# Kernel optimization log

Hardware: AMD Instinct MI355X
Metric: run time of the kernel (lower is better)

Reference implementation:

```python
import jax, jax.numpy as jnp
import numpy as np

K = 16          # NUM_PARTS (foreground parts); K+1 prototypes incl. background
D = 768         # EMBED_DIM
C = 200         # NUM_CLASSES
LN_EPS = 1e-6


def setup_inputs() -> dict:
    key = jax.random.key(0)
    k1, k2, k3, k4 = jax.random.split(key, 4)
    B, H, W = 32, 24, 24
    patch_features = jax.random.normal(k1, (B, H, W, D), dtype=jnp.float32)
    prototypes = 0.02 * jax.random.normal(k2, (K + 1, D), dtype=jnp.float32)
    ln_gamma = jnp.ones((D,), dtype=jnp.float32)
    ln_beta = jnp.zeros((D,), dtype=jnp.float32)
    # keras Dense default: glorot_uniform kernel, zero bias
    lim = np.sqrt(6.0 / (D + C)).astype(np.float32)
    w_cls = jax.random.uniform(k3, (D, C), dtype=jnp.float32, minval=-lim, maxval=lim)
    b_cls = jnp.zeros((C,), dtype=jnp.float32)
    return {
        "patch_features": patch_features,
        "prototypes": prototypes,
        "ln_gamma": ln_gamma,
        "ln_beta": ln_beta,
        "w_cls": w_cls,
        "b_cls": b_cls,
    }


def reference(patch_features, prototypes, ln_gamma, ln_beta, w_cls, b_cls):
    B, H, W, Dm = patch_features.shape
    P = H * W
    x = patch_features.reshape(B, P, Dm)                      # (B,P,D)

    # squared euclidean distance to K+1 prototypes, expressed as a GEMM:
    # ||z - p||^2 = ||z||^2 - 2 z.p + ||p||^2   -> (B,P,K+1)
    x_sq = jnp.sum(x * x, axis=-1, keepdims=True)             # (B,P,1)
    p_sq = jnp.sum(prototypes * prototypes, axis=-1)          # (K+1,)
    xp = jnp.einsum("bpd,kd->bpk", x, prototypes)             # (B,P,K+1)
    dists = x_sq - 2.0 * xp + p_sq                            # (B,P,K+1)

    # eval path: plain softmax over -distances
    a = jax.nn.softmax(-dists, axis=-1)                       # (B,P,K+1)

    # attention maps (B, K+1, H, W)
    A = jnp.transpose(a, (0, 2, 1)).reshape(B, K + 1, H, W)

    # weighted aggregation of patch features per part, normalized by P
    v_all = jnp.einsum("bpk,bpd->bkd", a, x) / jnp.float32(P) # (B,K+1,D)
    v_fg = v_all[:, :K, :]                                    # (B,K,D)

    # layernorm over last axis (eps=1e-6, learnable gamma/beta)
    mu = jnp.mean(v_fg, axis=-1, keepdims=True)
    var = jnp.mean(jnp.square(v_fg - mu), axis=-1, keepdims=True)
    v_norm = (v_fg - mu) * jax.lax.rsqrt(var + LN_EPS) * ln_gamma + ln_beta

    # shared per-part classifier + mean aggregation over parts
    logits_parts = jnp.einsum("bkd,dc->bkc", v_norm, w_cls) + b_cls  # (B,K,C)
    logits_agg = jnp.mean(logits_parts, axis=1)                      # (B,C)

    return (A, v_norm, logits_parts, logits_agg)
```

## Files before the change

### kernel.cpp

```cpp
#include <hip/hip_runtime.h>
#include <hip/hip_bf16.h>

#define B    32
#define P    576
#define D    768
#define K1   17
#define KFG  16
#define C    200
#define LN_EPS 1e-6f

typedef __attribute__((ext_vector_type(8))) short short8;
typedef __attribute__((ext_vector_type(4))) float f32x4;

__device__ inline unsigned short f2b(float f) {
    union { float f; unsigned u; } x; x.f = f;
    unsigned r = x.u + 0x7FFF + ((x.u >> 16) & 1);
    return (unsigned short)(r >> 16);
}

__device__ inline short8 cvt8(float4 a, float4 b) {
    union { unsigned u[4]; short8 s; } r;
    union { __hip_bfloat162 h; unsigned u; } c;
    c.h = __float22bfloat162_rn(make_float2(a.x, a.y)); r.u[0] = c.u;
    c.h = __float22bfloat162_rn(make_float2(a.z, a.w)); r.u[1] = c.u;
    c.h = __float22bfloat162_rn(make_float2(b.x, b.y)); r.u[2] = c.u;
    c.h = __float22bfloat162_rn(make_float2(b.z, b.w)); r.u[3] = c.u;
    return r.s;
}

__global__ __launch_bounds__(256) void k_pre(const float* __restrict__ proto,
                                             float* __restrict__ psq,
                                             unsigned short* __restrict__ pbf) {
    const int k = blockIdx.x, t = threadIdx.x;
    float a0 = proto[k * D + t], a1 = proto[k * D + t + 256], a2 = proto[k * D + t + 512];
    pbf[k * D + t]       = f2b(a0);
    pbf[k * D + t + 256] = f2b(a1);
    pbf[k * D + t + 512] = f2b(a2);
    float s = a0 * a0 + a1 * a1 + a2 * a2;
    #pragma unroll
    for (int o = 1; o < 64; o <<= 1) s += __shfl_xor(s, o, 64);
    __shared__ float r[4];
    if ((t & 63) == 0) r[t >> 6] = s;
    __syncthreads();
    if (t == 0) psq[k] = r[0] + r[1] + r[2] + r[3];
}

__global__ __launch_bounds__(64, 2) void k_dots(const float* __restrict__ x,
                                                const unsigned short* __restrict__ pbf,
                                                const float* __restrict__ psq,
                                                float* __restrict__ A_out,
                                                float* __restrict__ apool) {
    const int tile = blockIdx.x, b = blockIdx.y;
    const int lane = threadIdx.x;
    const int n = lane & 15, kq = lane >> 4;
    const int p0 = tile * 16;

    const float*          arow = x   + ((size_t)(b * P + p0 + n)) * D + kq * 8;
    const unsigned short* brow = pbf + (size_t)n  * D + kq * 8;
    const unsigned short* brw6 = pbf + (size_t)16 * D + kq * 8;

    f32x4 acc0 = {0.f, 0.f, 0.f, 0.f};
    f32x4 acc1 = {0.f, 0.f, 0.f, 0.f};

    #pragma unroll 8
    for (int s = 0; s < 24; ++s) {
        const float* ap = arow + s * 32;
        float4 v0 = *(const float4*)(ap);
        float4 v1 = *(const float4*)(ap + 4);
        short8 A  = cvt8(v0, v1);
        short8 Bv = *(const short8*)(brow + s * 32);
        short8 B6 = *(const short8*)(brw6 + s * 32);
        acc0 = __builtin_amdgcn_mfma_f32_16x16x32_bf16(A, Bv, acc0, 0, 0, 0);
        acc1 = __builtin_amdgcn_mfma_f32_16x16x32_bf16(A, B6, acc1, 0, 0, 0);
    }

    const float pq = psq[n], pq16 = psq[16];
    float a_[4], a16[4];
    #pragma unroll
    for (int r = 0; r < 4; ++r) {
        float l0  = 2.f * acc0[r] - pq;
        float l16 = 2.f * acc1[r] - pq16;
        float mx = l0;
        #pragma unroll
        for (int o = 1; o < 16; o <<= 1) mx = fmaxf(mx, __shfl_xor(mx, o, 64));
        mx = fmaxf(mx, l16);
        float e0  = __expf(l0 - mx);
        float e16 = __expf(l16 - mx);
        float sum = e0;
        #pragma unroll
        for (int o = 1; o < 16; o <<= 1) sum += __shfl_xor(sum, o, 64);
        sum += e16;
        const float inv = 1.f / sum;
        a_[r]  = e0 * inv;
        a16[r] = e16 * inv;
    }

    *(float4*)(A_out + ((size_t)b * K1 + n) * P + p0 + kq * 4) =
        make_float4(a_[0], a_[1], a_[2], a_[3]);
    if (n == 0)
        *(float4*)(A_out + ((size_t)b * K1 + 16) * P + p0 + kq * 4) =
            make_float4(a16[0], a16[1], a16[2], a16[3]);

    const float invP = 1.f / (float)P;
    #pragma unroll
    for (int r = 0; r < 4; ++r)
        apool[((size_t)b * P + p0 + kq * 4 + r) * KFG + n] = a_[r] * invP;
}

__global__ __launch_bounds__(256, 4) void k_pool(const float* __restrict__ x,
                                                 const float* __restrict__ apool,
                                                 float* __restrict__ vpart) {
    const int dc = blockIdx.x, psl = blockIdx.y, b = blockIdx.z;
    const int t = threadIdx.x;
    const int d = dc * 256 + t;

    const float* aw = apool + ((size_t)b * P + psl * 96) * KFG;
    const float* xp = x + ((size_t)b * P + psl * 96) * D + d;

    float acc[KFG];
    #pragma unroll
    for (int k = 0; k < KFG; ++k) acc[k] = 0.f;

    #pragma unroll 4
    for (int p = 0; p < 96; ++p) {
        float xv = xp[(size_t)p * D];
        f32x4 A0 = *(const f32x4*)(aw + p * 16);
        f32x4 A1 = *(const f32x4*)(aw + p * 16 + 4);
        f32x4 A2 = *(const f32x4*)(aw + p * 16 + 8);
        f32x4 A3 = *(const f32x4*)(aw + p * 16 + 12);
        acc[0]  += A0[0] * xv; acc[1]  += A0[1] * xv; acc[2]  += A0[2] * xv; acc[3]  += A0[3] * xv;
        acc[4]  += A1[0] * xv; acc[5]  += A1[1] * xv; acc[6]  += A1[2] * xv; acc[7]  += A1[3] * xv;
        acc[8]  += A2[0] * xv; acc[9]  += A2[1] * xv; acc[10] += A2[2] * xv; acc[11] += A2[3] * xv;
        acc[12] += A3[0] * xv; acc[13] += A3[1] * xv; acc[14] += A3[2] * xv; acc[15] += A3[3] * xv;
    }
    float* o = vpart + ((size_t)(psl * B + b) * KFG) * D + d;
    #pragma unroll
    for (int k = 0; k < KFG; ++k) o[(size_t)k * D] = acc[k];
}

__global__ __launch_bounds__(256) void k_ln(const float* __restrict__ vpart,
                                            const float* __restrict__ gamma,
                                            const float* __restrict__ beta,
                                            float* __restrict__ vnorm_out,
                                            float* __restrict__ vT) {
    const int k = blockIdx.x, b = blockIdx.y, t = threadIdx.x;
    const int lane = t & 63, wv = t >> 6;

    float v[3]; float s1 = 0.f, s2 = 0.f;
    #pragma unroll
    for (int j = 0; j < 3; ++j) {
        const int d = t + j * 256;
        float s = 0.f;
        #pragma unroll
        for (int psl = 0; psl < 6; ++psl)
            s += vpart[((size_t)(psl * B + b) * KFG + k) * D + d];
        v[j] = s; s1 += s; s2 += s * s;
    }
    #pragma unroll
    for (int o = 1; o < 64; o <<= 1) {
        s1 += __shfl_xor(s1, o, 64);
        s2 += __shfl_xor(s2, o, 64);
    }
    __shared__ float r1[4], r2[4];
    if (lane == 0) { r1[wv] = s1; r2[wv] = s2; }
    __syncthreads();
    s1 = r1[0] + r1[1] + r1[2] + r1[3];
    s2 = r2[0] + r2[1] + r2[2] + r2[3];

    const float mean = s1 * (1.f / (float)D);
    const float var  = s2 * (1.f / (float)D) - mean * mean;
    const float rs   = rsqrtf(var + LN_EPS);

    #pragma unroll
    for (int j = 0; j < 3; ++j) {
        const int d = t + j * 256;
        float vn = (v[j] - mean) * rs * gamma[d] + beta[d];
        vnorm_out[((size_t)b * KFG + k) * D + d] = vn;
        vT[((size_t)b * D + d) * KFG + k] = vn;
    }
}

__global__ __launch_bounds__(256) void k_cls(const float* __restrict__ vT,
                                             const float* __restrict__ W,
                                             float* __restrict__ lpart) {
    const int dq = blockIdx.x, b = blockIdx.y;
    const int c = threadIdx.x;
    const int cc = c < C ? c : (C - 1);

    const float* vt = vT + ((size_t)b * D + dq * 96) * KFG;
    const float* Wp = W + (size_t)dq * 96 * C + cc;

    float acc[KFG];
    #pragma unroll
    for (int k = 0; k < KFG; ++k) acc[k] = 0.f;

    #pragma unroll 4
    for (int i = 0; i < 96; ++i) {
        float wl = Wp[(size_t)i * C];
        f32x4 V0 = *(const f32x4*)(vt + i * 16);
        f32x4 V1 = *(const f32x4*)(vt + i * 16 + 4);
        f32x4 V2 = *(const f32x4*)(vt + i * 16 + 8);
        f32x4 V3 = *(const f32x4*)(vt + i * 16 + 12);
        acc[0]  += V0[0] * wl; acc[1]  += V0[1] * wl; acc[2]  += V0[2] * wl; acc[3]  += V0[3] * wl;
        acc[4]  += V1[0] * wl; acc[5]  += V1[1] * wl; acc[6]  += V1[2] * wl; acc[7]  += V1[3] * wl;
        acc[8]  += V2[0] * wl; acc[9]  += V2[1] * wl; acc[10] += V2[2] * wl; acc[11] += V2[3] * wl;
        acc[12] += V3[0] * wl; acc[13] += V3[1] * wl; acc[14] += V3[2] * wl; acc[15] += V3[3] * wl;
    }
    if (c < C) {
        float* o = lpart + ((size_t)(dq * B + b) * KFG) * C + c;
        #pragma unroll
        for (int k = 0; k < KFG; ++k) o[(size_t)k * C] = acc[k];
    }
}

__global__ __launch_bounds__(256) void k_comb(const float* __restrict__ lpart,
                                              const float* __restrict__ bcls,
                                              float* __restrict__ parts,
                                              float* __restrict__ agg) {
    const int b = blockIdx.x, c = threadIdx.x;
    if (c >= C) return;
    const float bc = bcls[c];
    float s_agg = 0.f;
    #pragma unroll
    for (int k = 0; k < KFG; ++k) {
        float s = bc;
        #pragma unroll
        for (int dq = 0; dq < 8; ++dq)
            s += lpart[((size_t)(dq * B + b) * KFG + k) * C + c];
        parts[((size_t)b * KFG + k) * C + c] = s;
        s_agg += s;
    }
    agg[(size_t)b * C + c] = s_agg * (1.f / (float)KFG);
}

extern "C" void kernel_launch(void* const* d_in, const int* in_sizes, int n_in,
                              void* d_out, int out_size, void* d_ws, size_t ws_size,
                              hipStream_t stream) {
    const float* x     = (const float*)d_in[0];
    const float* proto = (const float*)d_in[1];
    const float* gamma = (const float*)d_in[2];
    const float* beta  = (const float*)d_in[3];
    const float* W     = (const float*)d_in[4];
    const float* bcls  = (const float*)d_in[5];

    float* out = (float*)d_out;
    float* A_out     = out;
    float* vnorm_out = out + 313344;
    float* parts_out = out + 706560;
    float* agg_out   = out + 808960;

    float* ws = (float*)d_ws;
    float* psq  = ws;
    unsigned short* pbf = (unsigned short*)(ws + 32);
    float* apool = ws + 32 + 6528;
    float* vpart = apool + 294912;
    float* vT    = vpart + 2359296;
    float* lpart = vT + 393216;

    hipLaunchKernelGGL(k_pre,  dim3(K1),        dim3(256), 0, stream, proto, psq, pbf);
    hipLaunchKernelGGL(k_dots, dim3(36, B),     dim3(64),  0, stream, x, pbf, psq, A_out, apool);
    hipLaunchKernelGGL(k_pool, dim3(3, 6, B),   dim3(256), 0, stream, x, apool, vpart);
    hipLaunchKernelGGL(k_ln,   dim3(KFG, B),    dim3(256), 0, stream, vpart, gamma, beta, vnorm_out, vT);
    hipLaunchKernelGGL(k_cls,  dim3(8, B),      dim3(256), 0, stream, vT, W, lpart);
    hipLaunchKernelGGL(k_comb, dim3(B),         dim3(256), 0, stream, lpart, bcls, parts_out, agg_out);
}
```

Baseline: 147.8 us.

## Fuse all stages into one cooperative persistent kernel with grid syncs

Replaces the six separate kernel launches with a single cooperative kernel of 256 blocks that runs each stage in turn, separated by grid-wide barriers. The pooling stage now splits P into 8 slices instead of 6, and the workspace layout grows to match. The aim is to remove the per-launch gaps and tail effects between small stages. In exchange, the grid holds only 256 blocks of 256 threads, one block per CU, so the dots and pooling phases run at much lower occupancy than the original launches, and every grid barrier adds its own cost.

```diff
diff --git a/kernel.cpp b/kernel.cpp
--- a/kernel.cpp
+++ b/kernel.cpp
@@ -1,5 +1,8 @@
 #include <hip/hip_runtime.h>
 #include <hip/hip_bf16.h>
+#include <hip/hip_cooperative_groups.h>
+
+namespace cg = cooperative_groups;
 
 #define B    32
 #define P    576
@@ -28,209 +31,227 @@
     return r.s;
 }
 
-__global__ __launch_bounds__(256) void k_pre(const float* __restrict__ proto,
-                                             float* __restrict__ psq,
-                                             unsigned short* __restrict__ pbf) {
-    const int k = blockIdx.x, t = threadIdx.x;
-    float a0 = proto[k * D + t], a1 = proto[k * D + t + 256], a2 = proto[k * D + t + 512];
-    pbf[k * D + t]       = f2b(a0);
-    pbf[k * D + t + 256] = f2b(a1);
-    pbf[k * D + t + 512] = f2b(a2);
-    float s = a0 * a0 + a1 * a1 + a2 * a2;
-    #pragma unroll
-    for (int o = 1; o < 64; o <<= 1) s += __shfl_xor(s, o, 64);
-    __shared__ float r[4];
-    if ((t & 63) == 0) r[t >> 6] = s;
-    __syncthreads();
-    if (t == 0) psq[k] = r[0] + r[1] + r[2] + r[3];
-}
-
-__global__ __launch_bounds__(64, 2) void k_dots(const float* __restrict__ x,
-                                                const unsigned short* __restrict__ pbf,
-                                                const float* __restrict__ psq,
-                                                float* __restrict__ A_out,
-                                                float* __restrict__ apool) {
-    const int tile = blockIdx.x, b = blockIdx.y;
-    const int lane = threadIdx.x;
-    const int n = lane & 15, kq = lane >> 4;
-    const int p0 = tile * 16;
-
-    const float*          arow = x   + ((size_t)(b * P + p0 + n)) * D + kq * 8;
-    const unsigned short* brow = pbf + (size_t)n  * D + kq * 8;
-    const unsigned short* brw6 = pbf + (size_t)16 * D + kq * 8;
-
-    f32x4 acc0 = {0.f, 0.f, 0.f, 0.f};
-    f32x4 acc1 = {0.f, 0.f, 0.f, 0.f};
-
-    #pragma unroll 8
-    for (int s = 0; s < 24; ++s) {
-        const float* ap = arow + s * 32;
-        float4 v0 = *(const float4*)(ap);
-        float4 v1 = *(const float4*)(ap + 4);
-        short8 A  = cvt8(v0, v1);
-        short8 Bv = *(const short8*)(brow + s * 32);
-        short8 B6 = *(const short8*)(brw6 + s * 32);
-        acc0 = __builtin_amdgcn_mfma_f32_16x16x32_bf16(A, Bv, acc0, 0, 0, 0);
-        acc1 = __builtin_amdgcn_mfma_f32_16x16x32_bf16(A, B6, acc1, 0, 0, 0);
-    }
-
-    const float pq = psq[n], pq16 = psq[16];
-    float a_[4], a16[4];
-    #pragma unroll
-    for (int r = 0; r < 4; ++r) {
-        float l0  = 2.f * acc0[r] - pq;
-        float l16 = 2.f * acc1[r] - pq16;
-        float mx = l0;
+__global__ __launch_bounds__(256, 1) void k_all(
+        const float* __restrict__ x, const float* __restrict__ proto,
+        const float* __restrict__ gamma, const float* __restrict__ beta,
+        const float* __restrict__ W, const float* __restrict__ bcls,
+        float* __restrict__ A_out, float* __restrict__ vnorm_out,
+        float* __restrict__ parts_out, float* __restrict__ agg_out,
+        float* __restrict__ psq, unsigned short* __restrict__ pbf,
+        float* __restrict__ apool, float* __restrict__ vpart,
+        float* __restrict__ vT, float* __restrict__ lpart) {
+    cg::grid_group grid = cg::this_grid();
+    __shared__ float sred[8];
+
+    const int gid = blockIdx.x, t = threadIdx.x;
+    const int wv = t >> 6, lane = t & 63;
+
+    if (gid < K1) {
+        const int k = gid;
+        float a0 = proto[k * D + t], a1 = proto[k * D + t + 256], a2 = proto[k * D + t + 512];
+        pbf[k * D + t]       = f2b(a0);
+        pbf[k * D + t + 256] = f2b(a1);
+        pbf[k * D + t + 512] = f2b(a2);
+        float s = a0 * a0 + a1 * a1 + a2 * a2;
         #pragma unroll
-        for (int o = 1; o < 16; o <<= 1) mx = fmaxf(mx, __shfl_xor(mx, o, 64));
-        mx = fmaxf(mx, l16);
-        float e0  = __expf(l0 - mx);
-        float e16 = __expf(l16 - mx);
-        float sum = e0;
+        for (int o = 1; o < 64; o <<= 1) s += __shfl_xor(s, o, 64);
+        if (lane == 0) sred[wv] = s;
+        __syncthreads();
+        if (t == 0) psq[k] = sred[0] + sred[1] + sred[2] + sred[3];
+    }
+    __threadfence();
+    grid.sync();
+
+    {
+        const int n = lane & 15, kq = lane >> 4;
+        for (int u = gid * 4 + wv; u < 1152; u += 1024) {
+            const int tile = u % 36, b = u / 36;
+            const int p0 = tile * 16;
+
+            const float*          arow = x   + ((size_t)(b * P + p0 + n)) * D + kq * 8;
+            const unsigned short* brow = pbf + (size_t)n  * D + kq * 8;
+            const unsigned short* brw6 = pbf + (size_t)16 * D + kq * 8;
+
+            f32x4 acc0 = {0.f, 0.f, 0.f, 0.f};
+            f32x4 acc1 = {0.f, 0.f, 0.f, 0.f};
+
+            #pragma unroll 8
+            for (int s = 0; s < 24; ++s) {
+                const float* ap = arow + s * 32;
+                float4 v0 = *(const float4*)(ap);
+                float4 v1 = *(const float4*)(ap + 4);
+                short8 A  = cvt8(v0, v1);
+                short8 Bv = *(const short8*)(brow + s * 32);
+                short8 B6 = *(const short8*)(brw6 + s * 32);
+                acc0 = __builtin_amdgcn_mfma_f32_16x16x32_bf16(A, Bv, acc0, 0, 0, 0);
+                acc1 = __builtin_amdgcn_mfma_f32_16x16x32_bf16(A, B6, acc1, 0, 0, 0);
+            }
+
+            const float pq = psq[n], pq16 = psq[16];
+            float a_[4], a16[4];
+            #pragma unroll
+            for (int r = 0; r < 4; ++r) {
+                float l0  = 2.f * acc0[r] - pq;
+                float l16 = 2.f * acc1[r] - pq16;
+                float mx = l0;
+                #pragma unroll
+                for (int o = 1; o < 16; o <<= 1) mx = fmaxf(mx, __shfl_xor(mx, o, 64));
+                mx = fmaxf(mx, l16);
+                float e0  = __expf(l0 - mx);
+                float e16 = __expf(l16 - mx);
+                float sum = e0;
+                #pragma unroll
+                for (int o = 1; o < 16; o <<= 1) sum += __shfl_xor(sum, o, 64);
+                sum += e16;
+                const float inv = 1.f / sum;
+                a_[r]  = e0 * inv;
+                a16[r] = e16 * inv;
+            }
+
+            *(float4*)(A_out + ((size_t)b * K1 + n) * P + p0 + kq * 4) =
+                make_float4(a_[0], a_[1], a_[2], a_[3]);
+            if (n == 0)
+                *(float4*)(A_out + ((size_t)b * K1 + 16) * P + p0 + kq * 4) =
+                    make_float4(a16[0], a16[1], a16[2], a16[3]);
+
+            const float invP = 1.f / (float)P;
+            #pragma unroll
+            for (int r = 0; r < 4; ++r)
+                apool[((size_t)b * P + p0 + kq * 4 + r) * KFG + n] = a_[r] * invP;
+        }
+    }
+    __threadfence();
+    grid.sync();
+    __threadfence();
+
+    {
+        for (int u = gid; u < 768; u += 256) {
+            const int dc = u % 3, rem = u / 3;
+            const int psl = rem & 7, b = rem >> 3;
+            const int d = dc * 256 + t;
+
+            const float* aw = apool + ((size_t)b * P + psl * 72) * KFG;
+            const float* xp = x + ((size_t)b * P + psl * 72) * D + d;
+
+            float acc[KFG];
+            #pragma unroll
+            for (int k = 0; k < KFG; ++k) acc[k] = 0.f;
+
+            #pragma unroll 4
+            for (int p = 0; p < 72; ++p) {
+                float xv = xp[(size_t)p * D];
+                f32x4 A0 = *(const f32x4*)(aw + p * 16);
+                f32x4 A1 = *(const f32x4*)(aw + p * 16 + 4);
+                f32x4 A2 = *(const f32x4*)(aw + p * 16 + 8);
+                f32x4 A3 = *(const f32x4*)(aw + p * 16 + 12);
+                acc[0]  += A0[0] * xv; acc[1]  += A0[1] * xv; acc[2]  += A0[2] * xv; acc[3]  += A0[3] * xv;
+                acc[4]  += A1[0] * xv; acc[5]  += A1[1] * xv; acc[6]  += A1[2] * xv; acc[7]  += A1[3] * xv;
+                acc[8]  += A2[0] * xv; acc[9]  += A2[1] * xv; acc[10] += A2[2] * xv; acc[11] += A2[3] * xv;
+                acc[12] += A3[0] * xv; acc[13] += A3[1] * xv; acc[14] += A3[2] * xv; acc[15] += A3[3] * xv;
+            }
+            float* o = vpart + ((size_t)(psl * B + b) * KFG) * D + d;
+            #pragma unroll
+            for (int k = 0; k < KFG; ++k) o[(size_t)k * D] = acc[k];
+        }
+    }
+    __threadfence();
+    grid.sync();
+    __threadfence();
+
+    {
+        for (int rep = 0; rep < 2; ++rep) {
+            const int u = gid + rep * 256;
+            const int k = u & 15, b = u >> 4;
+
+            float v[3]; float s1 = 0.f, s2 = 0.f;
+            #pragma unroll
+            for (int j = 0; j < 3; ++j) {
+                const int d = t + j * 256;
+                float s = 0.f;
+                #pragma unroll
+                for (int psl = 0; psl < 8; ++psl)
+                    s += vpart[((size_t)(psl * B + b) * KFG + k) * D + d];
+                v[j] = s; s1 += s; s2 += s * s;
+            }
+            #pragma unroll
+            for (int o = 1; o < 64; o <<= 1) {
+                s1 += __shfl_xor(s1, o, 64);
+                s2 += __shfl_xor(s2, o, 64);
+            }
+            if (lane == 0) { sred[wv] = s1; sred[4 + wv] = s2; }
+            __syncthreads();
+            s1 = sred[0] + sred[1] + sred[2] + sred[3];
+            s2 = sred[4] + sred[5] + sred[6] + sred[7];
+            __syncthreads();
+
+            const float mean = s1 * (1.f / (float)D);
+            const float var  = s2 * (1.f / (float)D) - mean * mean;
+            const float rs   = rsqrtf(var + LN_EPS);
+
+            #pragma unroll
+            for (int j = 0; j < 3; ++j) {
+                const int d = t + j * 256;
+                float vn = (v[j] - mean) * rs * gamma[d] + beta[d];
+                vnorm_out[((size_t)b * KFG + k) * D + d] = vn;
+                vT[((size_t)b * D + d) * KFG + k] = vn;
+            }
+        }
+    }
+    __threadfence();
+    grid.sync();
+    __threadfence();
+
+    {
+        const int dq = gid & 7, b = gid >> 3;
+        const int c = t;
+        const int cc = c < C ? c : (C - 1);
+
+        const float* vt = vT + ((size_t)b * D + dq * 96) * KFG;
+        const float* Wp = W + (size_t)dq * 96 * C + cc;
+
+        float acc[KFG];
         #pragma unroll
-        for (int o = 1; o < 16; o <<= 1) sum += __shfl_xor(sum, o, 64);
-        sum += e16;
-        const float inv = 1.f / sum;
-        a_[r]  = e0 * inv;
-        a16[r] = e16 * inv;
-    }
-
-    *(float4*)(A_out + ((size_t)b * K1 + n) * P + p0 + kq * 4) =
-        make_float4(a_[0], a_[1], a_[2], a_[3]);
-    if (n == 0)
-        *(float4*)(A_out + ((size_t)b * K1 + 16) * P + p0 + kq * 4) =
-            make_float4(a16[0], a16[1], a16[2], a16[3]);
-
-    const float invP = 1.f / (float)P;
-    #pragma unroll
-    for (int r = 0; r < 4; ++r)
-        apool[((size_t)b * P + p0 + kq * 4 + r) * KFG + n] = a_[r] * invP;
-}
-
-__global__ __launch_bounds__(256, 4) void k_pool(const float* __restrict__ x,
-                                                 const float* __restrict__ apool,
-                                                 float* __restrict__ vpart) {
-    const int dc = blockIdx.x, psl = blockIdx.y, b = blockIdx.z;
-    const int t = threadIdx.x;
-    const int d = dc * 256 + t;
-
-    const float* aw = apool + ((size_t)b * P + psl * 96) * KFG;
-    const float* xp = x + ((size_t)b * P + psl * 96) * D + d;
-
-    float acc[KFG];
-    #pragma unroll
-    for (int k = 0; k < KFG; ++k) acc[k] = 0.f;
-
-    #pragma unroll 4
-    for (int p = 0; p < 96; ++p) {
-        float xv = xp[(size_t)p * D];
-        f32x4 A0 = *(const f32x4*)(aw + p * 16);
-        f32x4 A1 = *(const f32x4*)(aw + p * 16 + 4);
-        f32x4 A2 = *(const f32x4*)(aw + p * 16 + 8);
-        f32x4 A3 = *(const f32x4*)(aw + p * 16 + 12);
-        acc[0]  += A0[0] * xv; acc[1]  += A0[1] * xv; acc[2]  += A0[2] * xv; acc[3]  += A0[3] * xv;
-        acc[4]  += A1[0] * xv; acc[5]  += A1[1] * xv; acc[6]  += A1[2] * xv; acc[7]  += A1[3] * xv;
-        acc[8]  += A2[0] * xv; acc[9]  += A2[1] * xv; acc[10] += A2[2] * xv; acc[11] += A2[3] * xv;
-        acc[12] += A3[0] * xv; acc[13] += A3[1] * xv; acc[14] += A3[2] * xv; acc[15] += A3[3] * xv;
-    }
-    float* o = vpart + ((size_t)(psl * B + b) * KFG) * D + d;
-    #pragma unroll
-    for (int k = 0; k < KFG; ++k) o[(size_t)k * D] = acc[k];
-}
-
-__global__ __launch_bounds__(256) void k_ln(const float* __restrict__ vpart,
-                                            const float* __restrict__ gamma,
-                                            const float* __restrict__ beta,
-                                            float* __restrict__ vnorm_out,
-                                            float* __restrict__ vT) {
-    const int k = blockIdx.x, b = blockIdx.y, t = threadIdx.x;
-    const int lane = t & 63, wv = t >> 6;
-
-    float v[3]; float s1 = 0.f, s2 = 0.f;
-    #pragma unroll
-    for (int j = 0; j < 3; ++j) {
-        const int d = t + j * 256;
-        float s = 0.f;
-        #pragma unroll
-        for (int psl = 0; psl < 6; ++psl)
-            s += vpart[((size_t)(psl * B + b) * KFG + k) * D + d];
-        v[j] = s; s1 += s; s2 += s * s;
-    }
-    #pragma unroll
-    for (int o = 1; o < 64; o <<= 1) {
-        s1 += __shfl_xor(s1, o, 64);
-        s2 += __shfl_xor(s2, o, 64);
-    }
-    __shared__ float r1[4], r2[4];
-    if (lane == 0) { r1[wv] = s1; r2[wv] = s2; }
-    __syncthreads();
-    s1 = r1[0] + r1[1] + r1[2] + r1[3];
-    s2 = r2[0] + r2[1] + r2[2] + r2[3];
-
-    const float mean = s1 * (1.f / (float)D);
-    const float var  = s2 * (1.f / (float)D) - mean * mean;
-    const float rs   = rsqrtf(var + LN_EPS);
-
-    #pragma unroll
-    for (int j = 0; j < 3; ++j) {
-        const int d = t + j * 256;
-        float vn = (v[j] - mean) * rs * gamma[d] + beta[d];
-        vnorm_out[((size_t)b * KFG + k) * D + d] = vn;
-        vT[((size_t)b * D + d) * KFG + k] = vn;
-    }
-}
-
-__global__ __launch_bounds__(256) void k_cls(const float* __restrict__ vT,
-                                             const float* __restrict__ W,
-                                             float* __restrict__ lpart) {
-    const int dq = blockIdx.x, b = blockIdx.y;
-    const int c = threadIdx.x;
-    const int cc = c < C ? c : (C - 1);
-
-    const float* vt = vT + ((size_t)b * D + dq * 96) * KFG;
-    const float* Wp = W + (size_t)dq * 96 * C + cc;
-
-    float acc[KFG];
-    #pragma unroll
-    for (int k = 0; k < KFG; ++k) acc[k] = 0.f;
-
-    #pragma unroll 4
-    for (int i = 0; i < 96; ++i) {
-        float wl = Wp[(size_t)i * C];
-        f32x4 V0 = *(const f32x4*)(vt + i * 16);
-        f32x4 V1 = *(const f32x4*)(vt + i * 16 + 4);
-        f32x4 V2 = *(const f32x4*)(vt + i * 16 + 8);
-        f32x4 V3 = *(const f32x4*)(vt + i * 16 + 12);
-        acc[0]  += V0[0] * wl; acc[1]  += V0[1] * wl; acc[2]  += V0[2] * wl; acc[3]  += V0[3] * wl;
-        acc[4]  += V1[0] * wl; acc[5]  += V1[1] * wl; acc[6]  += V1[2] * wl; acc[7]  += V1[3] * wl;
-        acc[8]  += V2[0] * wl; acc[9]  += V2[1] * wl; acc[10] += V2[2] * wl; acc[11] += V2[3] * wl;
-        acc[12] += V3[0] * wl; acc[13] += V3[1] * wl; acc[14] += V3[2] * wl; acc[15] += V3[3] * wl;
-    }
-    if (c < C) {
-        float* o = lpart + ((size_t)(dq * B + b) * KFG) * C + c;
-        #pragma unroll
-        for (int k = 0; k < KFG; ++k) o[(size_t)k * C] = acc[k];
-    }
-}
-
-__global__ __launch_bounds__(256) void k_comb(const float* __restrict__ lpart,
-                                              const float* __restrict__ bcls,
-                                              float* __restrict__ parts,
-                                              float* __restrict__ agg) {
-    const int b = blockIdx.x, c = threadIdx.x;
-    if (c >= C) return;
-    const float bc = bcls[c];
-    float s_agg = 0.f;
-    #pragma unroll
-    for (int k = 0; k < KFG; ++k) {
-        float s = bc;
-        #pragma unroll
-        for (int dq = 0; dq < 8; ++dq)
-            s += lpart[((size_t)(dq * B + b) * KFG + k) * C + c];
-        parts[((size_t)b * KFG + k) * C + c] = s;
-        s_agg += s;
-    }
-    agg[(size_t)b * C + c] = s_agg * (1.f / (float)KFG);
+        for (int k = 0; k < KFG; ++k) acc[k] = 0.f;
+
+        #pragma unroll 4
+        for (int i = 0; i < 96; ++i) {
+            float wl = Wp[(size_t)i * C];
+            f32x4 V0 = *(const f32x4*)(vt + i * 16);
+            f32x4 V1 = *(const f32x4*)(vt + i * 16 + 4);
+            f32x4 V2 = *(const f32x4*)(vt + i * 16 + 8);
+            f32x4 V3 = *(const f32x4*)(vt + i * 16 + 12);
+            acc[0]  += V0[0] * wl; acc[1]  += V0[1] * wl; acc[2]  += V0[2] * wl; acc[3]  += V0[3] * wl;
+            acc[4]  += V1[0] * wl; acc[5]  += V1[1] * wl; acc[6]  += V1[2] * wl; acc[7]  += V1[3] * wl;
+            acc[8]  += V2[0] * wl; acc[9]  += V2[1] * wl; acc[10] += V2[2] * wl; acc[11] += V2[3] * wl;
+            acc[12] += V3[0] * wl; acc[13] += V3[1] * wl; acc[14] += V3[2] * wl; acc[15] += V3[3] * wl;
+        }
+        if (c < C) {
+            float* o = lpart + ((size_t)(dq * B + b) * KFG) * C + c;
+            #pragma unroll
+            for (int k = 0; k < KFG; ++k) o[(size_t)k * C] = acc[k];
+        }
+    }
+    __threadfence();
+    grid.sync();
+    __threadfence();
+
+    if (gid < B) {
+        const int b = gid, c = t;
+        if (c < C) {
+            const float bc = bcls[c];
+            float s_agg = 0.f;
+            #pragma unroll
+            for (int k = 0; k < KFG; ++k) {
+                float s = bc;
+                #pragma unroll
+                for (int dq = 0; dq < 8; ++dq)
+                    s += lpart[((size_t)(dq * B + b) * KFG + k) * C + c];
+                parts_out[((size_t)b * KFG + k) * C + c] = s;
+                s_agg += s;
+            }
+            agg_out[(size_t)b * C + c] = s_agg * (1.f / (float)KFG);
+        }
+    }
 }
 
 extern "C" void kernel_launch(void* const* d_in, const int* in_sizes, int n_in,
@@ -254,13 +275,13 @@
     unsigned short* pbf = (unsigned short*)(ws + 32);
     float* apool = ws + 32 + 6528;
     float* vpart = apool + 294912;
-    float* vT    = vpart + 2359296;
+    float* vT    = vpart + 3145728;
     float* lpart = vT + 393216;
 
-    hipLaunchKernelGGL(k_pre,  dim3(K1),        dim3(256), 0, stream, proto, psq, pbf);
-    hipLaunchKernelGGL(k_dots, dim3(36, B),     dim3(64),  0, stream, x, pbf, psq, A_out, apool);
-    hipLaunchKernelGGL(k_pool, dim3(3, 6, B),   dim3(256), 0, stream, x, apool, vpart);
-    hipLaunchKernelGGL(k_ln,   dim3(KFG, B),    dim3(256), 0, stream, vpart, gamma, beta, vnorm_out, vT);
-    hipLaunchKernelGGL(k_cls,  dim3(8, B),      dim3(256), 0, stream, vT, W, lpart);
-    hipLaunchKernelGGL(k_comb, dim3(B),         dim3(256), 0, stream, lpart, bcls, parts_out, agg_out);
-}
+    void* args[] = { (void*)&x, (void*)&proto, (void*)&gamma, (void*)&beta,
+                     (void*)&W, (void*)&bcls,
+                     (void*)&A_out, (void*)&vnorm_out, (void*)&parts_out, (void*)&agg_out,
+                     (void*)&psq, (void*)&pbf, (void*)&apool, (void*)&vpart,
+                     (void*)&vT, (void*)&lpart };
+    hipLaunchCooperativeKernel((void*)k_all, dim3(256), dim3(256), args, 0, stream);
+}
```

Result: slower. 520.6 us (+252.1%).

## Fuse distance, softmax and pooling; fuse layernorm, classifier and combine with flags

Applied to the files above, without the earlier changes.

Collapses six launches into two. The front kernel folds prototype conversion and norms into the distance MFMA loop, keeps attention weights in shared memory, and pools its own 64-patch slice of x while that slice is likely still in cache. The back kernel has one block per batch run LayerNorm and publish a flag; the other classifier blocks spin on it, and a ticket counter lets the last block combine the partial logits. This removes launch gaps and the second full trip of x through HBM, but adds spin-waiting, heavy register use for the pooling accumulators, and fewer blocks during pooling.

```diff
diff --git a/kernel.cpp b/kernel.cpp
--- a/kernel.cpp
+++ b/kernel.cpp
@@ -11,12 +11,6 @@
 
 typedef __attribute__((ext_vector_type(8))) short short8;
 typedef __attribute__((ext_vector_type(4))) float f32x4;
-
-__device__ inline unsigned short f2b(float f) {
-    union { float f; unsigned u; } x; x.f = f;
-    unsigned r = x.u + 0x7FFF + ((x.u >> 16) & 1);
-    return (unsigned short)(r >> 16);
-}
 
 __device__ inline short8 cvt8(float4 a, float4 b) {
     union { unsigned u[4]; short8 s; } r;
@@ -27,59 +21,56 @@
     c.h = __float22bfloat162_rn(make_float2(b.z, b.w)); r.u[3] = c.u;
     return r.s;
 }
-
-__global__ __launch_bounds__(256) void k_pre(const float* __restrict__ proto,
-                                             float* __restrict__ psq,
-                                             unsigned short* __restrict__ pbf) {
-    const int k = blockIdx.x, t = threadIdx.x;
-    float a0 = proto[k * D + t], a1 = proto[k * D + t + 256], a2 = proto[k * D + t + 512];
-    pbf[k * D + t]       = f2b(a0);
-    pbf[k * D + t + 256] = f2b(a1);
-    pbf[k * D + t + 512] = f2b(a2);
-    float s = a0 * a0 + a1 * a1 + a2 * a2;
-    #pragma unroll
-    for (int o = 1; o < 64; o <<= 1) s += __shfl_xor(s, o, 64);
-    __shared__ float r[4];
-    if ((t & 63) == 0) r[t >> 6] = s;
-    __syncthreads();
-    if (t == 0) psq[k] = r[0] + r[1] + r[2] + r[3];
-}
-
-__global__ __launch_bounds__(64, 2) void k_dots(const float* __restrict__ x,
-                                                const unsigned short* __restrict__ pbf,
-                                                const float* __restrict__ psq,
-                                                float* __restrict__ A_out,
-                                                float* __restrict__ apool) {
-    const int tile = blockIdx.x, b = blockIdx.y;
-    const int lane = threadIdx.x;
+__device__ inline float sq8(float4 a, float4 b) {
+    return a.x*a.x + a.y*a.y + a.z*a.z + a.w*a.w
+         + b.x*b.x + b.y*b.y + b.z*b.z + b.w*b.w;
+}
+
+__global__ __launch_bounds__(256) void k_front(const float* __restrict__ x,
+                                               const float* __restrict__ proto,
+                                               float* __restrict__ A_out,
+                                               float* __restrict__ vpart,
+                                               int* __restrict__ flags) {
+    __shared__ float as_[64 * 16];
+    const int psl = blockIdx.x, b = blockIdx.y;
+    const int t = threadIdx.x, wv = t >> 6, lane = t & 63;
     const int n = lane & 15, kq = lane >> 4;
-    const int p0 = tile * 16;
-
-    const float*          arow = x   + ((size_t)(b * P + p0 + n)) * D + kq * 8;
-    const unsigned short* brow = pbf + (size_t)n  * D + kq * 8;
-    const unsigned short* brw6 = pbf + (size_t)16 * D + kq * 8;
+    const int p0 = psl * 64 + wv * 16;
+
+    if (psl == 0 && b == 0 && t < 64) flags[t] = 0;
+
+    const float* arow = x     + ((size_t)(b * P + p0 + n)) * D + kq * 8;
+    const float* brow = proto + (size_t)n  * D + kq * 8;
+    const float* brw6 = proto + (size_t)16 * D + kq * 8;
 
     f32x4 acc0 = {0.f, 0.f, 0.f, 0.f};
     f32x4 acc1 = {0.f, 0.f, 0.f, 0.f};
+    float sq0 = 0.f, sq6 = 0.f;
 
     #pragma unroll 8
     for (int s = 0; s < 24; ++s) {
-        const float* ap = arow + s * 32;
-        float4 v0 = *(const float4*)(ap);
-        float4 v1 = *(const float4*)(ap + 4);
-        short8 A  = cvt8(v0, v1);
-        short8 Bv = *(const short8*)(brow + s * 32);
-        short8 B6 = *(const short8*)(brw6 + s * 32);
+        float4 a0 = *(const float4*)(arow + s * 32);
+        float4 a1 = *(const float4*)(arow + s * 32 + 4);
+        float4 b0 = *(const float4*)(brow + s * 32);
+        float4 b1 = *(const float4*)(brow + s * 32 + 4);
+        float4 c0 = *(const float4*)(brw6 + s * 32);
+        float4 c1 = *(const float4*)(brw6 + s * 32 + 4);
+        short8 A  = cvt8(a0, a1);
+        short8 Bv = cvt8(b0, b1);
+        short8 B6 = cvt8(c0, c1);
+        sq0 += sq8(b0, b1);
+        sq6 += sq8(c0, c1);
         acc0 = __builtin_amdgcn_mfma_f32_16x16x32_bf16(A, Bv, acc0, 0, 0, 0);
         acc1 = __builtin_amdgcn_mfma_f32_16x16x32_bf16(A, B6, acc1, 0, 0, 0);
     }
-
-    const float pq = psq[n], pq16 = psq[16];
+    sq0 += __shfl_xor(sq0, 16, 64); sq0 += __shfl_xor(sq0, 32, 64);
+    sq6 += __shfl_xor(sq6, 16, 64); sq6 += __shfl_xor(sq6, 32, 64);
+
     float a_[4], a16[4];
     #pragma unroll
     for (int r = 0; r < 4; ++r) {
-        float l0  = 2.f * acc0[r] - pq;
-        float l16 = 2.f * acc1[r] - pq16;
+        float l0  = 2.f * acc0[r] - sq0;
+        float l16 = 2.f * acc1[r] - sq6;
         float mx = l0;
         #pragma unroll
         for (int o = 1; o < 16; o <<= 1) mx = fmaxf(mx, __shfl_xor(mx, o, 64));
@@ -104,89 +95,101 @@
     const float invP = 1.f / (float)P;
     #pragma unroll
     for (int r = 0; r < 4; ++r)
-        apool[((size_t)b * P + p0 + kq * 4 + r) * KFG + n] = a_[r] * invP;
-}
-
-__global__ __launch_bounds__(256, 4) void k_pool(const float* __restrict__ x,
-                                                 const float* __restrict__ apool,
-                                                 float* __restrict__ vpart) {
-    const int dc = blockIdx.x, psl = blockIdx.y, b = blockIdx.z;
-    const int t = threadIdx.x;
-    const int d = dc * 256 + t;
-
-    const float* aw = apool + ((size_t)b * P + psl * 96) * KFG;
-    const float* xp = x + ((size_t)b * P + psl * 96) * D + d;
-
-    float acc[KFG];
-    #pragma unroll
-    for (int k = 0; k < KFG; ++k) acc[k] = 0.f;
-
-    #pragma unroll 4
-    for (int p = 0; p < 96; ++p) {
-        float xv = xp[(size_t)p * D];
-        f32x4 A0 = *(const f32x4*)(aw + p * 16);
-        f32x4 A1 = *(const f32x4*)(aw + p * 16 + 4);
-        f32x4 A2 = *(const f32x4*)(aw + p * 16 + 8);
-        f32x4 A3 = *(const f32x4*)(aw + p * 16 + 12);
-        acc[0]  += A0[0] * xv; acc[1]  += A0[1] * xv; acc[2]  += A0[2] * xv; acc[3]  += A0[3] * xv;
-        acc[4]  += A1[0] * xv; acc[5]  += A1[1] * xv; acc[6]  += A1[2] * xv; acc[7]  += A1[3] * xv;
-        acc[8]  += A2[0] * xv; acc[9]  += A2[1] * xv; acc[10] += A2[2] * xv; acc[11] += A2[3] * xv;
-        acc[12] += A3[0] * xv; acc[13] += A3[1] * xv; acc[14] += A3[2] * xv; acc[15] += A3[3] * xv;
-    }
-    float* o = vpart + ((size_t)(psl * B + b) * KFG) * D + d;
-    #pragma unroll
-    for (int k = 0; k < KFG; ++k) o[(size_t)k * D] = acc[k];
-}
-
-__global__ __launch_bounds__(256) void k_ln(const float* __restrict__ vpart,
-                                            const float* __restrict__ gamma,
-                                            const float* __restrict__ beta,
-                                            float* __restrict__ vnorm_out,
-                                            float* __restrict__ vT) {
-    const int k = blockIdx.x, b = blockIdx.y, t = threadIdx.x;
-    const int lane = t & 63, wv = t >> 6;
-
-    float v[3]; float s1 = 0.f, s2 = 0.f;
-    #pragma unroll
-    for (int j = 0; j < 3; ++j) {
-        const int d = t + j * 256;
-        float s = 0.f;
-        #pragma unroll
-        for (int psl = 0; psl < 6; ++psl)
-            s += vpart[((size_t)(psl * B + b) * KFG + k) * D + d];
-        v[j] = s; s1 += s; s2 += s * s;
-    }
-    #pragma unroll
-    for (int o = 1; o < 64; o <<= 1) {
-        s1 += __shfl_xor(s1, o, 64);
-        s2 += __shfl_xor(s2, o, 64);
-    }
-    __shared__ float r1[4], r2[4];
-    if (lane == 0) { r1[wv] = s1; r2[wv] = s2; }
+        as_[(wv * 16 + kq * 4 + r) * KFG + n] = a_[r] * invP;
     __syncthreads();
-    s1 = r1[0] + r1[1] + r1[2] + r1[3];
-    s2 = r2[0] + r2[1] + r2[2] + r2[3];
-
-    const float mean = s1 * (1.f / (float)D);
-    const float var  = s2 * (1.f / (float)D) - mean * mean;
-    const float rs   = rsqrtf(var + LN_EPS);
-
-    #pragma unroll
-    for (int j = 0; j < 3; ++j) {
-        const int d = t + j * 256;
-        float vn = (v[j] - mean) * rs * gamma[d] + beta[d];
-        vnorm_out[((size_t)b * KFG + k) * D + d] = vn;
-        vT[((size_t)b * D + d) * KFG + k] = vn;
-    }
-}
-
-__global__ __launch_bounds__(256) void k_cls(const float* __restrict__ vT,
-                                             const float* __restrict__ W,
-                                             float* __restrict__ lpart) {
-    const int dq = blockIdx.x, b = blockIdx.y;
-    const int c = threadIdx.x;
+
+    float accp[3][KFG];
+    #pragma unroll
+    for (int j = 0; j < 3; ++j)
+        #pragma unroll
+        for (int k = 0; k < KFG; ++k) accp[j][k] = 0.f;
+
+    const float* xb = x + ((size_t)(b * P + psl * 64)) * D;
+    for (int p = 0; p < 64; ++p) {
+        f32x4 A0 = *(const f32x4*)(as_ + p * 16);
+        f32x4 A1 = *(const f32x4*)(as_ + p * 16 + 4);
+        f32x4 A2 = *(const f32x4*)(as_ + p * 16 + 8);
+        f32x4 A3 = *(const f32x4*)(as_ + p * 16 + 12);
+        float av[KFG] = { A0[0],A0[1],A0[2],A0[3], A1[0],A1[1],A1[2],A1[3],
+                          A2[0],A2[1],A2[2],A2[3], A3[0],A3[1],A3[2],A3[3] };
+        #pragma unroll
+        for (int j = 0; j < 3; ++j) {
+            float xv = xb[(size_t)p * D + t + j * 256];
+            #pragma unroll
+            for (int k = 0; k < KFG; ++k) accp[j][k] += av[k] * xv;
+        }
+    }
+    float* o = vpart + ((size_t)(psl * B + b) * KFG) * D;
+    #pragma unroll
+    for (int j = 0; j < 3; ++j)
+        #pragma unroll
+        for (int k = 0; k < KFG; ++k)
+            o[(size_t)k * D + t + j * 256] = accp[j][k];
+}
+
+__global__ __launch_bounds__(256) void k_back(const float* __restrict__ vpart,
+                                              const float* __restrict__ gamma,
+                                              const float* __restrict__ beta,
+                                              const float* __restrict__ W,
+                                              const float* __restrict__ bcls,
+                                              float* __restrict__ vnorm_out,
+                                              float* __restrict__ vT,
+                                              float* __restrict__ lpart,
+                                              float* __restrict__ parts_out,
+                                              float* __restrict__ agg_out,
+                                              int* __restrict__ flags) {
+    const int dq = blockIdx.x & 7, b = blockIdx.x >> 3;
+    const int t = threadIdx.x, wv = t >> 6, lane = t & 63;
+    int* lnflag = flags;
+    int* ticket = flags + 32;
+
+    if (dq == 0) {
+        #pragma unroll
+        for (int kk = 0; kk < 4; ++kk) {
+            const int k = wv * 4 + kk;
+            float v[12]; float s1 = 0.f, s2 = 0.f;
+            #pragma unroll
+            for (int i = 0; i < 12; ++i) {
+                const int d = i * 64 + lane;
+                float s = 0.f;
+                #pragma unroll
+                for (int psl = 0; psl < 9; ++psl)
+                    s += vpart[((size_t)(psl * B + b) * KFG + k) * D + d];
+                v[i] = s; s1 += s; s2 += s * s;
+            }
+            #pragma unroll
+            for (int o = 1; o < 64; o <<= 1) {
+                s1 += __shfl_xor(s1, o, 64);
+                s2 += __shfl_xor(s2, o, 64);
+            }
+            const float mean = s1 * (1.f / (float)D);
+            const float var  = s2 * (1.f / (float)D) - mean * mean;
+            const float rs   = rsqrtf(var + LN_EPS);
+            #pragma unroll
+            for (int i = 0; i < 12; ++i) {
+                const int d = i * 64 + lane;
+                float vn = (v[i] - mean) * rs * gamma[d] + beta[d];
+                vnorm_out[((size_t)b * KFG + k) * D + d] = vn;
+                vT[((size_t)b * D + d) * KFG + k] = vn;
+            }
+        }
+        __syncthreads();
+        if (t == 0) {
+            __builtin_amdgcn_fence(__ATOMIC_RELEASE, "agent");
+            __hip_atomic_store(&lnflag[b], 1, __ATOMIC_RELAXED, __HIP_MEMORY_SCOPE_AGENT);
+        }
+    } else {
+        if (t == 0) {
+            while (__hip_atomic_load(&lnflag[b], __ATOMIC_RELAXED,
+                                     __HIP_MEMORY_SCOPE_AGENT) == 0)
+                __builtin_amdgcn_s_sleep(8);
+        }
+        __syncthreads();
+        __builtin_amdgcn_fence(__ATOMIC_ACQUIRE, "agent");
+    }
+
+    const int c = t;
     const int cc = c < C ? c : (C - 1);
-
     const float* vt = vT + ((size_t)b * D + dq * 96) * KFG;
     const float* Wp = W + (size_t)dq * 96 * C + cc;
 
@@ -211,26 +214,32 @@
         #pragma unroll
         for (int k = 0; k < KFG; ++k) o[(size_t)k * C] = acc[k];
     }
-}
-
-__global__ __launch_bounds__(256) void k_comb(const float* __restrict__ lpart,
-                                              const float* __restrict__ bcls,
-                                              float* __restrict__ parts,
-                                              float* __restrict__ agg) {
-    const int b = blockIdx.x, c = threadIdx.x;
-    if (c >= C) return;
-    const float bc = bcls[c];
-    float s_agg = 0.f;
-    #pragma unroll
-    for (int k = 0; k < KFG; ++k) {
-        float s = bc;
-        #pragma unroll
-        for (int dq = 0; dq < 8; ++dq)
-            s += lpart[((size_t)(dq * B + b) * KFG + k) * C + c];
-        parts[((size_t)b * KFG + k) * C + c] = s;
-        s_agg += s;
-    }
-    agg[(size_t)b * C + c] = s_agg * (1.f / (float)KFG);
+    __syncthreads();
+
+    __shared__ int swin;
+    if (t == 0) {
+        __builtin_amdgcn_fence(__ATOMIC_RELEASE, "agent");
+        swin = __hip_atomic_fetch_add(&ticket[b], 1, __ATOMIC_RELAXED,
+                                      __HIP_MEMORY_SCOPE_AGENT);
+    }
+    __syncthreads();
+    if (swin == 7) {
+        __builtin_amdgcn_fence(__ATOMIC_ACQUIRE, "agent");
+        if (c < C) {
+            const float bc = bcls[c];
+            float s_agg = 0.f;
+            #pragma unroll
+            for (int k = 0; k < KFG; ++k) {
+                float s = bc;
+                #pragma unroll
+                for (int q = 0; q < 8; ++q)
+                    s += lpart[((size_t)(q * B + b) * KFG + k) * C + c];
+                parts_out[((size_t)b * KFG + k) * C + c] = s;
+                s_agg += s;
+            }
+            agg_out[(size_t)b * C + c] = s_agg * (1.f / (float)KFG);
+        }
+    }
 }
 
 extern "C" void kernel_launch(void* const* d_in, const int* in_sizes, int n_in,
@@ -250,17 +259,14 @@
     float* agg_out   = out + 808960;
 
     float* ws = (float*)d_ws;
-    float* psq  = ws;
-    unsigned short* pbf = (unsigned short*)(ws + 32);
-    float* apool = ws + 32 + 6528;
-    float* vpart = apool + 294912;
-    float* vT    = vpart + 2359296;
+    float* vpart = ws;
+    float* vT    = vpart + 3538944;
     float* lpart = vT + 393216;
-
-    hipLaunchKernelGGL(k_pre,  dim3(K1),        dim3(256), 0, stream, proto, psq, pbf);
-    hipLaunchKernelGGL(k_dots, dim3(36, B),     dim3(64),  0, stream, x, pbf, psq, A_out, apool);
-    hipLaunchKernelGGL(k_pool, dim3(3, 6, B),   dim3(256), 0, stream, x, apool, vpart);
-    hipLaunchKernelGGL(k_ln,   dim3(KFG, B),    dim3(256), 0, stream, vpart, gamma, beta, vnorm_out, vT);
-    hipLaunchKernelGGL(k_cls,  dim3(8, B),      dim3(256), 0, stream, vT, W, lpart);
-    hipLaunchKernelGGL(k_comb, dim3(B),         dim3(256), 0, stream, lpart, bcls, parts_out, agg_out);
-}
+    int*   flags = (int*)(lpart + 819200);
+
+    hipLaunchKernelGGL(k_front, dim3(9, B), dim3(256), 0, stream,
+                       x, proto, A_out, vpart, flags);
+    hipLaunchKernelGGL(k_back,  dim3(256),  dim3(256), 0, stream,
+                       vpart, gamma, beta, W, bcls,
+                       vnorm_out, vT, lpart, parts_out, agg_out, flags);
+}
```

Result: slower. 195.9 us (+32.5%).

## Fuse prototype prep into dots kernel and split D across four waves

Applied to the files above, without the earlier changes.

Removes the separate prototype preprocessing kernel: k_dots now loads fp32 prototypes directly, converts them to bf16 in-register, and computes prototype squared norms on the fly. The dots kernel grows from one wave to four waves per block, each handling a quarter of D, with partial accumulators reduced through shared memory before wave 0 does the softmax. This cuts one launch and shortens the serial MFMA chain per block, at the cost of redundant prototype loads and conversions in every block plus an LDS reduction and barrier.

```diff
diff --git a/kernel.cpp b/kernel.cpp
--- a/kernel.cpp
+++ b/kernel.cpp
@@ -11,12 +11,6 @@
 
 typedef __attribute__((ext_vector_type(8))) short short8;
 typedef __attribute__((ext_vector_type(4))) float f32x4;
-
-__device__ inline unsigned short f2b(float f) {
-    union { float f; unsigned u; } x; x.f = f;
-    unsigned r = x.u + 0x7FFF + ((x.u >> 16) & 1);
-    return (unsigned short)(r >> 16);
-}
 
 __device__ inline short8 cvt8(float4 a, float4 b) {
     union { unsigned u[4]; short8 s; } r;
@@ -27,59 +21,73 @@
     c.h = __float22bfloat162_rn(make_float2(b.z, b.w)); r.u[3] = c.u;
     return r.s;
 }
-
-__global__ __launch_bounds__(256) void k_pre(const float* __restrict__ proto,
-                                             float* __restrict__ psq,
-                                             unsigned short* __restrict__ pbf) {
-    const int k = blockIdx.x, t = threadIdx.x;
-    float a0 = proto[k * D + t], a1 = proto[k * D + t + 256], a2 = proto[k * D + t + 512];
-    pbf[k * D + t]       = f2b(a0);
-    pbf[k * D + t + 256] = f2b(a1);
-    pbf[k * D + t + 512] = f2b(a2);
-    float s = a0 * a0 + a1 * a1 + a2 * a2;
-    #pragma unroll
-    for (int o = 1; o < 64; o <<= 1) s += __shfl_xor(s, o, 64);
-    __shared__ float r[4];
-    if ((t & 63) == 0) r[t >> 6] = s;
-    __syncthreads();
-    if (t == 0) psq[k] = r[0] + r[1] + r[2] + r[3];
-}
-
-__global__ __launch_bounds__(64, 2) void k_dots(const float* __restrict__ x,
-                                                const unsigned short* __restrict__ pbf,
-                                                const float* __restrict__ psq,
-                                                float* __restrict__ A_out,
-                                                float* __restrict__ apool) {
+__device__ inline float sq8(float4 a, float4 b) {
+    return a.x*a.x + a.y*a.y + a.z*a.z + a.w*a.w
+         + b.x*b.x + b.y*b.y + b.z*b.z + b.w*b.w;
+}
+
+__global__ __launch_bounds__(256) void k_dots(const float* __restrict__ x,
+                                              const float* __restrict__ proto,
+                                              float* __restrict__ A_out,
+                                              float* __restrict__ apool) {
+    __shared__ float scL[4 * 64 * 11];
     const int tile = blockIdx.x, b = blockIdx.y;
-    const int lane = threadIdx.x;
+    const int t = threadIdx.x, wv = t >> 6, lane = t & 63;
     const int n = lane & 15, kq = lane >> 4;
     const int p0 = tile * 16;
 
-    const float*          arow = x   + ((size_t)(b * P + p0 + n)) * D + kq * 8;
-    const unsigned short* brow = pbf + (size_t)n  * D + kq * 8;
-    const unsigned short* brw6 = pbf + (size_t)16 * D + kq * 8;
+    const float* arow = x     + ((size_t)(b * P + p0 + n)) * D + wv * 192 + kq * 8;
+    const float* brow = proto + (size_t)n  * D + wv * 192 + kq * 8;
+    const float* brw6 = proto + (size_t)16 * D + wv * 192 + kq * 8;
 
     f32x4 acc0 = {0.f, 0.f, 0.f, 0.f};
     f32x4 acc1 = {0.f, 0.f, 0.f, 0.f};
-
-    #pragma unroll 8
-    for (int s = 0; s < 24; ++s) {
-        const float* ap = arow + s * 32;
-        float4 v0 = *(const float4*)(ap);
-        float4 v1 = *(const float4*)(ap + 4);
-        short8 A  = cvt8(v0, v1);
-        short8 Bv = *(const short8*)(brow + s * 32);
-        short8 B6 = *(const short8*)(brw6 + s * 32);
+    float sq0 = 0.f, sq6 = 0.f;
+
+    #pragma unroll
+    for (int s = 0; s < 6; ++s) {
+        float4 a0 = *(const float4*)(arow + s * 32);
+        float4 a1 = *(const float4*)(arow + s * 32 + 4);
+        float4 b0 = *(const float4*)(brow + s * 32);
+        float4 b1 = *(const float4*)(brow + s * 32 + 4);
+        float4 c0 = *(const float4*)(brw6 + s * 32);
+        float4 c1 = *(const float4*)(brw6 + s * 32 + 4);
+        short8 A  = cvt8(a0, a1);
+        short8 Bv = cvt8(b0, b1);
+        short8 B6 = cvt8(c0, c1);
+        sq0 += sq8(b0, b1);
+        sq6 += sq8(c0, c1);
         acc0 = __builtin_amdgcn_mfma_f32_16x16x32_bf16(A, Bv, acc0, 0, 0, 0);
         acc1 = __builtin_amdgcn_mfma_f32_16x16x32_bf16(A, B6, acc1, 0, 0, 0);
     }
-
-    const float pq = psq[n], pq16 = psq[16];
+    sq0 += __shfl_xor(sq0, 16, 64); sq0 += __shfl_xor(sq0, 32, 64);
+    sq6 += __shfl_xor(sq6, 16, 64); sq6 += __shfl_xor(sq6, 32, 64);
+
+    {
+        float* s = scL + (wv * 64 + lane) * 11;
+        #pragma unroll
+        for (int r = 0; r < 4; ++r) { s[r] = acc0[r]; s[r + 4] = acc1[r]; }
+        s[8] = sq0; s[9] = sq6;
+    }
+    __syncthreads();
+    if (wv != 0) return;
+
+    float f0[4], f1[4]; float fsq0 = 0.f, fsq6 = 0.f;
+    #pragma unroll
+    for (int r = 0; r < 4; ++r) { f0[r] = 0.f; f1[r] = 0.f; }
+    #pragma unroll
+    for (int w = 0; w < 4; ++w) {
+        const float* s = scL + (w * 64 + lane) * 11;
+        #pragma unroll
+        for (int r = 0; r < 4; ++r) { f0[r] += s[r]; f1[r] += s[r + 4]; }
+        fsq0 += s[8]; fsq6 += s[9];
+    }
+
     float a_[4], a16[4];
     #pragma unroll
     for (int r = 0; r < 4; ++r) {
-        float l0  = 2.f * acc0[r] - pq;
-        float l16 = 2.f * acc1[r] - pq16;
+        float l0  = 2.f * f0[r] - fsq0;
+        float l16 = 2.f * f1[r] - fsq6;
         float mx = l0;
         #pragma unroll
         for (int o = 1; o < 16; o <<= 1) mx = fmaxf(mx, __shfl_xor(mx, o, 64));
@@ -250,17 +258,14 @@
     float* agg_out   = out + 808960;
 
     float* ws = (float*)d_ws;
-    float* psq  = ws;
-    unsigned short* pbf = (unsigned short*)(ws + 32);
-    float* apool = ws + 32 + 6528;
+    float* apool = ws;
     float* vpart = apool + 294912;
     float* vT    = vpart + 2359296;
     float* lpart = vT + 393216;
 
-    hipLaunchKernelGGL(k_pre,  dim3(K1),        dim3(256), 0, stream, proto, psq, pbf);
-    hipLaunchKernelGGL(k_dots, dim3(36, B),     dim3(64),  0, stream, x, pbf, psq, A_out, apool);
-    hipLaunchKernelGGL(k_pool, dim3(3, 6, B),   dim3(256), 0, stream, x, apool, vpart);
-    hipLaunchKernelGGL(k_ln,   dim3(KFG, B),    dim3(256), 0, stream, vpart, gamma, beta, vnorm_out, vT);
-    hipLaunchKernelGGL(k_cls,  dim3(8, B),      dim3(256), 0, stream, vT, W, lpart);
-    hipLaunchKernelGGL(k_comb, dim3(B),         dim3(256), 0, stream, lpart, bcls, parts_out, agg_out);
-}
+    hipLaunchKernelGGL(k_dots, dim3(36, B),   dim3(256), 0, stream, x, proto, A_out, apool);
+    hipLaunchKernelGGL(k_pool, dim3(3, 6, B), dim3(256), 0, stream, x, apool, vpart);
+    hipLaunchKernelGGL(k_ln,   dim3(KFG, B),  dim3(256), 0, stream, vpart, gamma, beta, vnorm_out, vT);
+    hipLaunchKernelGGL(k_cls,  dim3(8, B),    dim3(256), 0, stream, vT, W, lpart);
+    hipLaunchKernelGGL(k_comb, dim3(B),       dim3(256), 0, stream, lpart, bcls, parts_out, agg_out);
+}
```

Result: faster. 139.3 us (-5.8%).
